# Kernel tuning notes

Measured on AMD Instinct MI355X. Metric: run time of the kernel, lower is better.

## Reference

```python
import jax, jax.numpy as jnp
import numpy as np

NSITES, NUP, NDN, BATCH = 256, 128, 128, 4096

def setup_inputs() -> dict:
    key = jax.random.key(0)
    k1, k2, k3, k4, k5 = jax.random.split(key, 5)
    phi_up = jax.random.normal(k1, (NSITES, NUP), dtype=jnp.float32)
    phi_dn = jax.random.normal(k2, (NSITES, NDN), dtype=jnp.float32)
    nfmodes = 2 * NSITES
    v = jax.random.normal(k3, (nfmodes, nfmodes), dtype=jnp.float32) / nfmodes
    # occupation: exactly NUP ones in first NSITES slots, NDN ones in last NSITES
    base_up = jnp.concatenate([jnp.ones(NUP, jnp.int32), jnp.zeros(NSITES - NUP, jnp.int32)])
    base_dn = jnp.concatenate([jnp.ones(NDN, jnp.int32), jnp.zeros(NSITES - NDN, jnp.int32)])
    n_up = jax.vmap(lambda k: jax.random.permutation(k, base_up))(jax.random.split(k4, BATCH))
    n_dn = jax.vmap(lambda k: jax.random.permutation(k, base_dn))(jax.random.split(k5, BATCH))
    n = jnp.concatenate([n_up, n_dn], axis=1)  # [B, 2*nsites]
    return {"n": n, "phi_up": phi_up, "phi_dn": phi_dn, "v": v}

def reference(n, phi_up, phi_dn, v):
    nsites, nup = phi_up.shape
    nf = n.astype(phi_up.dtype)                       # [B, 2*nsites]
    # Jastrow log factor: -0.5 * n @ v @ n  (sign is +1)
    log_j = -0.5 * jnp.einsum('bi,ij,bj->b', nf, v, nf)
    # fermion_idx: sorted indices of occupied modes, split by spin sector.
    # stable argsort of -n gives occupied indices in ascending order.
    idx_up = jnp.argsort(-n[:, :nsites], axis=1)[:, :nup]          # [B, nup]
    idx_dn = jnp.argsort(-n[:, nsites:], axis=1)[:, :phi_dn.shape[1]]
    M_up = phi_up[idx_up]                             # [B, nup, nup]
    M_dn = phi_dn[idx_dn]                             # [B, ndn, ndn]
    sign_up, logabs_up = jnp.linalg.slogdet(M_up)
    sign_dn, logabs_dn = jnp.linalg.slogdet(M_dn)
    sign = sign_up * sign_dn                          # jastrow sign is ones
    logabs = log_j + logabs_up + logabs_dn
    return jnp.stack([sign, logabs], axis=0)          # [2, B]
```

## Files before the change

kernel.cpp:

```cpp
#include <hip/hip_runtime.h>
#include <hip/hip_bf16.h>

#define NSITES 256
#define NM 128
#define NMODES 512

typedef unsigned long long u64;
typedef unsigned int u32;

#define REP8(M)    M(0) M(1) M(2) M(3) M(4) M(5) M(6) M(7)
#define REP8P(M,P) M(0,P) M(1,P) M(2,P) M(3,P) M(4,P) M(5,P) M(6,P) M(7,P)

template<int CTRL>
__device__ __forceinline__ float dpp_max(float x) {
  const int xi = __float_as_int(x);
  const int yi = __builtin_amdgcn_update_dpp(xi, xi, CTRL, 0xF, 0xF, false);
  return fmaxf(x, __int_as_float(yi));
}
__device__ __forceinline__ float wave_max(float x) {
  x = dpp_max<0x128>(x);
  x = dpp_max<0x124>(x);
  x = dpp_max<0x122>(x);
  x = dpp_max<0x121>(x);
  x = dpp_max<0x142>(x);
  x = dpp_max<0x143>(x);
  return __int_as_float(__builtin_amdgcn_readlane(__float_as_int(x), 63));
}

__global__ __launch_bounds__(256, 2) void lu_kernel(
    const int* __restrict__ n, const float* __restrict__ phi_up,
    const float* __restrict__ phi_dn, float* __restrict__ ws, int B)
{
  __shared__ int occ[NSITES];
  __shared__ int wcnt[4];
  __shared__ float colbuf[2][NM];
  __shared__ float rowP[2][NM];
  __shared__ int ipiv[NM];

  const int t = threadIdx.x;
  const int tx = t & 15, ty = t >> 4;
  const int lane = t & 63, wv = t >> 6;
  const int bs = blockIdx.x;
  const int b = bs >> 1, spin = bs & 1;
  const int* nn = n + b * NMODES + spin * NSITES;
  const float* phi = spin ? phi_dn : phi_up;

  {
    int v = nn[t];
    u64 m = __ballot(v != 0);
    if (lane == 0) wcnt[wv] = __popcll(m);
    __syncthreads();
    int off = 0;
    for (int w = 0; w < wv; ++w) off += wcnt[w];
    if (v) occ[off + __popcll(m & ((1ull << lane) - 1))] = t;
    __syncthreads();
  }

  float a[8][8];
#define GATH(II) { const float* pr_ = phi + occ[(II)*16 + ty] * NM; \
  a[II][0] = pr_[0*16+tx]; a[II][1] = pr_[1*16+tx]; \
  a[II][2] = pr_[2*16+tx]; a[II][3] = pr_[3*16+tx]; \
  a[II][4] = pr_[4*16+tx]; a[II][5] = pr_[5*16+tx]; \
  a[II][6] = pr_[6*16+tx]; a[II][7] = pr_[7*16+tx]; }
  REP8(GATH)
#undef GATH

  if (tx == 0) {
#define PUB0(II) colbuf[0][(II)*16 + ty] = a[II][0];
    REP8(PUB0)
#undef PUB0
  }
  if (tx == 1) {
#define PUB1(II) colbuf[1][(II)*16 + ty] = a[II][0];
    REP8(PUB1)
#undef PUB1
  }
  __syncthreads();

  float c1 = colbuf[0][lane];
  float c2 = colbuf[0][lane + 64];
  int r1 = 0, r2 = 0;
  float l2sum = 0.f;
  int sb = 0;
  const int bidx0 = (ty) << 2;
  const int bidx1 = (16 + ty) << 2;
  const int bidx2 = (32 + ty) << 2;
  const int bidx3 = (48 + ty) << 2;

  for (int k = 0; k < NM; ++k) {
    const int cur = k & 1;

    const float ca1 = r1 ? -1.0f : fabsf(c1);
    const float ca2 = r2 ? -1.0f : fabsf(c2);
    const float mx = wave_max(fmaxf(ca1, ca2));
    const u64 b1m = __ballot(ca1 == mx);
    const u64 b2m = __ballot(ca2 == mx);
    int p = b1m ? (__ffsll(b1m) - 1) : (__ffsll(b2m) + 63);
    p = __builtin_amdgcn_readfirstlane(p);
    const int pb = p >> 4, pt = p & 15, pl = p & 63;
    const float pivv = __int_as_float(
        p < 64 ? __builtin_amdgcn_readlane(__float_as_int(c1), pl)
               : __builtin_amdgcn_readlane(__float_as_int(c2), pl));
    const float rpiv = 1.0f / pivv;
    r1 |= (p == lane);
    r2 |= (p == lane + 64);
    const float m1 = r1 ? 0.f : c1 * rpiv;
    const float m2 = r2 ? 0.f : c2 * rpiv;

    if (ty == pt) {
      switch (pb) {
#define SRP(II) case II: \
  rowP[cur][0*16+tx]=a[II][0]; rowP[cur][1*16+tx]=a[II][1]; \
  rowP[cur][2*16+tx]=a[II][2]; rowP[cur][3*16+tx]=a[II][3]; \
  rowP[cur][4*16+tx]=a[II][4]; rowP[cur][5*16+tx]=a[II][5]; \
  rowP[cur][6*16+tx]=a[II][6]; rowP[cur][7*16+tx]=a[II][7]; break;
        REP8(SRP)
#undef SRP
      }
    }
    if (t == 0) ipiv[k] = p;
    l2sum += __log2f(mx);
    sb ^= (int)(__float_as_uint(pivv) >> 31);

    __syncthreads();

    if (k < NM - 1) {
      float mI[8];
#define BPM(II) mI[II] = __int_as_float(__builtin_amdgcn_ds_bpermute( \
    (II) < 4 ? ((II)==0?bidx0:(II)==1?bidx1:(II)==2?bidx2:bidx3) \
             : ((II)==4?bidx0:(II)==5?bidx1:(II)==6?bidx2:bidx3), \
    __float_as_int((II) < 4 ? m1 : m2)));
      REP8(BPM)
#undef BPM

      const int T = (k + 1) >> 4;
      float pr[8];
#define PRE(JJ, KB) if ((JJ) >= (KB)) pr[JJ] = rowP[cur][(JJ)*16 + tx];
#define UPDROW(II, KB) { \
  if (0 >= (KB)) a[II][0] = fmaf(-mI[II], pr[0], a[II][0]); \
  if (1 >= (KB)) a[II][1] = fmaf(-mI[II], pr[1], a[II][1]); \
  if (2 >= (KB)) a[II][2] = fmaf(-mI[II], pr[2], a[II][2]); \
  if (3 >= (KB)) a[II][3] = fmaf(-mI[II], pr[3], a[II][3]); \
  if (4 >= (KB)) a[II][4] = fmaf(-mI[II], pr[4], a[II][4]); \
  if (5 >= (KB)) a[II][5] = fmaf(-mI[II], pr[5], a[II][5]); \
  if (6 >= (KB)) a[II][6] = fmaf(-mI[II], pr[6], a[II][6]); \
  if (7 >= (KB)) a[II][7] = fmaf(-mI[II], pr[7], a[II][7]); }
#define LUCASE(KB) case KB: { REP8P(PRE, KB) REP8P(UPDROW, KB) } break;
      switch (T) {
        REP8(LUCASE)
      }
#undef LUCASE
#undef UPDROW
#undef PRE

      float d1 = colbuf[cur ^ 1][lane];
      float d2 = colbuf[cur ^ 1][lane + 64];
      const float ud = __int_as_float(
          p < 64 ? __builtin_amdgcn_readlane(__float_as_int(d1), pl)
                 : __builtin_amdgcn_readlane(__float_as_int(d2), pl));
      c1 = fmaf(-m1, ud, d1);
      c2 = fmaf(-m2, ud, d2);

      if (k < NM - 2) {
        const int cn = k + 2;
        if (tx == (cn & 15)) {
          switch (cn >> 4) {
#define PUBC(JJ) case JJ: \
  colbuf[cur][0*16+ty]=a[0][JJ]; colbuf[cur][1*16+ty]=a[1][JJ]; \
  colbuf[cur][2*16+ty]=a[2][JJ]; colbuf[cur][3*16+ty]=a[3][JJ]; \
  colbuf[cur][4*16+ty]=a[4][JJ]; colbuf[cur][5*16+ty]=a[5][JJ]; \
  colbuf[cur][6*16+ty]=a[6][JJ]; colbuf[cur][7*16+ty]=a[7][JJ]; break;
            REP8(PUBC)
#undef PUBC
          }
        }
      }
    }
  }

  __syncthreads();
  int inv = 0;
  if (t < NM) {
    const int my = ipiv[t];
    for (int l = t + 1; l < NM; ++l) inv += (my > ipiv[l]) ? 1 : 0;
  }
  const u64 bal = __ballot((t < NM) && (inv & 1));
  if (lane == 0) wcnt[wv] = __popcll(bal);
  __syncthreads();

  if (t == 0) {
    const int par = (wcnt[0] + wcnt[1] + wcnt[2] + wcnt[3]) & 1;
    const int s = (sb ^ par) & 1;
    ws[B + spin * B + b] = l2sum * 0.6931471805599453f;
    ws[3 * B + spin * B + b] = s ? -1.f : 1.f;
  }
}

__global__ __launch_bounds__(256) void jastrow_kernel(
    const int* __restrict__ n, const float* __restrict__ v,
    float* __restrict__ ws, int B)
{
  __shared__ int occ[256];
  __shared__ float nf[NMODES];
  __shared__ int wcnt[8];
  __shared__ float red[256];
  const int t = threadIdx.x, b = blockIdx.x;
  const int lane = t & 63, wv = t >> 6;
  const int* nn = n + b * NMODES;
  int v0 = nn[t], v1 = nn[256 + t];
  nf[t] = (float)v0;
  nf[256 + t] = (float)v1;
  u64 m0 = __ballot(v0 != 0), m1 = __ballot(v1 != 0);
  if (lane == 0) { wcnt[wv] = __popcll(m0); wcnt[4 + wv] = __popcll(m1); }
  __syncthreads();
  int off0 = 0;
  for (int w = 0; w < wv; ++w) off0 += wcnt[w];
  int base1 = wcnt[0] + wcnt[1] + wcnt[2] + wcnt[3];
  int off1 = base1;
  for (int w = 0; w < wv; ++w) off1 += wcnt[4 + w];
  if (v0) occ[off0 + __popcll(m0 & ((1ull << lane) - 1))] = t;
  if (v1) occ[off1 + __popcll(m1 & ((1ull << lane) - 1))] = 256 + t;
  __syncthreads();

  float acc = 0.f;
  for (int r = wv * 64; r < wv * 64 + 64; ++r) {
    const float* row = v + occ[r] * NMODES;
#pragma unroll
    for (int cc = 0; cc < 8; ++cc) {
      int c = cc * 64 + lane;
      acc += row[c] * nf[c];
    }
  }
  red[t] = acc;
  __syncthreads();
  for (int s = 128; s >= 1; s >>= 1) {
    if (t < s) red[t] += red[t + s];
    __syncthreads();
  }
  if (t == 0) ws[b] = -0.5f * red[0];
}

__global__ void finalize_kernel(const float* __restrict__ ws,
                                float* __restrict__ out, int B)
{
  int b = blockIdx.x * 256 + threadIdx.x;
  if (b < B) {
    float lj = ws[b];
    float la_u = ws[B + b], la_d = ws[2 * B + b];
    float s_u = ws[3 * B + b], s_d = ws[4 * B + b];
    out[b] = s_u * s_d;
    out[B + b] = lj + la_u + la_d;
  }
}

extern "C" void kernel_launch(void* const* d_in, const int* in_sizes, int n_in,
                              void* d_out, int out_size, void* d_ws, size_t ws_size,
                              hipStream_t stream) {
  const int* n = (const int*)d_in[0];
  const float* phi_up = (const float*)d_in[1];
  const float* phi_dn = (const float*)d_in[2];
  const float* v = (const float*)d_in[3];
  float* out = (float*)d_out;
  float* ws = (float*)d_ws;
  const int B = in_sizes[0] / NMODES;

  jastrow_kernel<<<B, 256, 0, stream>>>(n, v, ws, B);
  lu_kernel<<<2 * B, 256, 0, stream>>>(n, phi_up, phi_dn, ws, B);
  finalize_kernel<<<(B + 255) / 256, 256, 0, stream>>>(ws, out, B);
}
```

Baseline: 1.634 ms.

## Process two pivot columns per step in LU to halve block barriers

Restructures the per-matrix LU loop to factor two pivot steps per iteration: both pivots are chosen in registers from the two lookahead columns, the multipliers are corrected for the row coupling, and the trailing matrix gets a rank-2 update. This halves the number of __syncthreads and shared-memory round trips per factorization and fuses two FMA passes over the register tile. It adds extra bpermutes, readlanes and a deeper column lookahead, and uses the approximate rcp intrinsic instead of exact division for the pivot reciprocal, which may slightly change precision.

```diff
diff --git a/kernel.cpp b/kernel.cpp
--- a/kernel.cpp
+++ b/kernel.cpp
@@ -4,6 +4,7 @@
 #define NSITES 256
 #define NM 128
 #define NMODES 512
+#define NS 64
 
 typedef unsigned long long u64;
 typedef unsigned int u32;
@@ -26,6 +27,11 @@
   x = dpp_max<0x143>(x);
   return __int_as_float(__builtin_amdgcn_readlane(__float_as_int(x), 63));
 }
+__device__ __forceinline__ float rl2(float x1, float x2, int p) {
+  const int v1 = __builtin_amdgcn_readlane(__float_as_int(x1), p & 63);
+  const int v2 = __builtin_amdgcn_readlane(__float_as_int(x2), p & 63);
+  return __int_as_float(p < 64 ? v1 : v2);
+}
 
 __global__ __launch_bounds__(256, 2) void lu_kernel(
     const int* __restrict__ n, const float* __restrict__ phi_up,
@@ -33,8 +39,8 @@
 {
   __shared__ int occ[NSITES];
   __shared__ int wcnt[4];
-  __shared__ float colbuf[2][NM];
-  __shared__ float rowP[2][NM];
+  __shared__ float colbuf[2][2][NM];
+  __shared__ float rowP[2][2][NM];
   __shared__ int ipiv[NM];
 
   const int t = threadIdx.x;
@@ -65,20 +71,16 @@
   REP8(GATH)
 #undef GATH
 
-  if (tx == 0) {
-#define PUB0(II) colbuf[0][(II)*16 + ty] = a[II][0];
-    REP8(PUB0)
-#undef PUB0
-  }
-  if (tx == 1) {
-#define PUB1(II) colbuf[1][(II)*16 + ty] = a[II][0];
-    REP8(PUB1)
-#undef PUB1
-  }
-  __syncthreads();
-
-  float c1 = colbuf[0][lane];
-  float c2 = colbuf[0][lane + 64];
+#define PUBP(II, DST) DST[(II)*16 + ty] = a[II][0];
+  if (tx == 0) { float* d_ = &colbuf[1][0][0]; REP8P(PUBP, d_) }
+  if (tx == 1) { float* d_ = &colbuf[1][1][0]; REP8P(PUBP, d_) }
+  if (tx == 2) { float* d_ = &colbuf[0][0][0]; REP8P(PUBP, d_) }
+  if (tx == 3) { float* d_ = &colbuf[0][1][0]; REP8P(PUBP, d_) }
+#undef PUBP
+  __syncthreads();
+
+  float c1 = colbuf[1][0][lane], c2 = colbuf[1][0][lane + 64];
+  float d1 = colbuf[1][1][lane], d2 = colbuf[1][1][lane + 64];
   int r1 = 0, r2 = 0;
   float l2sum = 0.f;
   int sb = 0;
@@ -87,92 +89,127 @@
   const int bidx2 = (32 + ty) << 2;
   const int bidx3 = (48 + ty) << 2;
 
-  for (int k = 0; k < NM; ++k) {
-    const int cur = k & 1;
+  for (int s = 0; s < NS; ++s) {
+    const int pp = s & 1;
+    const int k0 = 2 * s;
 
     const float ca1 = r1 ? -1.0f : fabsf(c1);
     const float ca2 = r2 ? -1.0f : fabsf(c2);
-    const float mx = wave_max(fmaxf(ca1, ca2));
-    const u64 b1m = __ballot(ca1 == mx);
-    const u64 b2m = __ballot(ca2 == mx);
-    int p = b1m ? (__ffsll(b1m) - 1) : (__ffsll(b2m) + 63);
-    p = __builtin_amdgcn_readfirstlane(p);
-    const int pb = p >> 4, pt = p & 15, pl = p & 63;
-    const float pivv = __int_as_float(
-        p < 64 ? __builtin_amdgcn_readlane(__float_as_int(c1), pl)
-               : __builtin_amdgcn_readlane(__float_as_int(c2), pl));
-    const float rpiv = 1.0f / pivv;
-    r1 |= (p == lane);
-    r2 |= (p == lane + 64);
-    const float m1 = r1 ? 0.f : c1 * rpiv;
-    const float m2 = r2 ? 0.f : c2 * rpiv;
-
-    if (ty == pt) {
-      switch (pb) {
-#define SRP(II) case II: \
-  rowP[cur][0*16+tx]=a[II][0]; rowP[cur][1*16+tx]=a[II][1]; \
-  rowP[cur][2*16+tx]=a[II][2]; rowP[cur][3*16+tx]=a[II][3]; \
-  rowP[cur][4*16+tx]=a[II][4]; rowP[cur][5*16+tx]=a[II][5]; \
-  rowP[cur][6*16+tx]=a[II][6]; rowP[cur][7*16+tx]=a[II][7]; break;
-        REP8(SRP)
-#undef SRP
+    const float mx1 = wave_max(fmaxf(ca1, ca2));
+    const u64 A1 = __ballot(ca1 == mx1);
+    const u64 A2 = __ballot(ca2 == mx1);
+    int p1 = A1 ? (__ffsll(A1) - 1) : (__ffsll(A2) + 63);
+    p1 = __builtin_amdgcn_readfirstlane(p1);
+    const float piv1 = rl2(c1, c2, p1);
+    const float rp1 = __builtin_amdgcn_rcpf(piv1);
+    r1 |= (p1 == lane);
+    r2 |= (p1 == lane + 64);
+    const float m1a = r1 ? 0.f : c1 * rp1;
+    const float m1b = r2 ? 0.f : c2 * rp1;
+
+    const float ud = rl2(d1, d2, p1);
+    d1 = fmaf(-m1a, ud, d1);
+    d2 = fmaf(-m1b, ud, d2);
+
+    const float da1 = r1 ? -1.0f : fabsf(d1);
+    const float da2 = r2 ? -1.0f : fabsf(d2);
+    const float mx2 = wave_max(fmaxf(da1, da2));
+    const u64 B1 = __ballot(da1 == mx2);
+    const u64 B2 = __ballot(da2 == mx2);
+    int p2 = B1 ? (__ffsll(B1) - 1) : (__ffsll(B2) + 63);
+    p2 = __builtin_amdgcn_readfirstlane(p2);
+    const float piv2 = rl2(d1, d2, p2);
+    const float rp2 = __builtin_amdgcn_rcpf(piv2);
+    r1 |= (p2 == lane);
+    r2 |= (p2 == lane + 64);
+    const float m2a = r1 ? 0.f : d1 * rp2;
+    const float m2b = r2 ? 0.f : d2 * rp2;
+    const float mp = rl2(m1a, m1b, p2);
+
+    const int pb1 = p1 >> 4, pt1 = p1 & 15;
+    const int pb2 = p2 >> 4, pt2 = p2 & 15;
+#define SRX(II, DST) case II: \
+  DST[0*16+tx]=a[II][0]; DST[1*16+tx]=a[II][1]; DST[2*16+tx]=a[II][2]; DST[3*16+tx]=a[II][3]; \
+  DST[4*16+tx]=a[II][4]; DST[5*16+tx]=a[II][5]; DST[6*16+tx]=a[II][6]; DST[7*16+tx]=a[II][7]; break;
+    if (s < NS - 1) {
+      if (ty == pt1) {
+        float* d_ = &rowP[pp][0][0];
+        switch (pb1) { REP8P(SRX, d_) }
       }
-    }
-    if (t == 0) ipiv[k] = p;
-    l2sum += __log2f(mx);
-    sb ^= (int)(__float_as_uint(pivv) >> 31);
+      if (ty == pt2) {
+        float* d_ = &rowP[pp][1][0];
+        switch (pb2) { REP8P(SRX, d_) }
+      }
+    }
+#undef SRX
+    if (t == 0) { ipiv[k0] = p1; ipiv[k0 + 1] = p2; }
+    l2sum += __log2f(mx1) + __log2f(mx2);
+    sb ^= (int)((__float_as_uint(piv1) ^ __float_as_uint(piv2)) >> 31);
 
     __syncthreads();
-
-    if (k < NM - 1) {
-      float mI[8];
-#define BPM(II) mI[II] = __int_as_float(__builtin_amdgcn_ds_bpermute( \
-    (II) < 4 ? ((II)==0?bidx0:(II)==1?bidx1:(II)==2?bidx2:bidx3) \
-             : ((II)==4?bidx0:(II)==5?bidx1:(II)==6?bidx2:bidx3), \
-    __float_as_int((II) < 4 ? m1 : m2)));
-      REP8(BPM)
-#undef BPM
-
-      const int T = (k + 1) >> 4;
-      float pr[8];
-#define PRE(JJ, KB) if ((JJ) >= (KB)) pr[JJ] = rowP[cur][(JJ)*16 + tx];
-#define UPDROW(II, KB) { \
-  if (0 >= (KB)) a[II][0] = fmaf(-mI[II], pr[0], a[II][0]); \
-  if (1 >= (KB)) a[II][1] = fmaf(-mI[II], pr[1], a[II][1]); \
-  if (2 >= (KB)) a[II][2] = fmaf(-mI[II], pr[2], a[II][2]); \
-  if (3 >= (KB)) a[II][3] = fmaf(-mI[II], pr[3], a[II][3]); \
-  if (4 >= (KB)) a[II][4] = fmaf(-mI[II], pr[4], a[II][4]); \
-  if (5 >= (KB)) a[II][5] = fmaf(-mI[II], pr[5], a[II][5]); \
-  if (6 >= (KB)) a[II][6] = fmaf(-mI[II], pr[6], a[II][6]); \
-  if (7 >= (KB)) a[II][7] = fmaf(-mI[II], pr[7], a[II][7]); }
-#define LUCASE(KB) case KB: { REP8P(PRE, KB) REP8P(UPDROW, KB) } break;
-      switch (T) {
-        REP8(LUCASE)
-      }
-#undef LUCASE
-#undef UPDROW
-#undef PRE
-
-      float d1 = colbuf[cur ^ 1][lane];
-      float d2 = colbuf[cur ^ 1][lane + 64];
-      const float ud = __int_as_float(
-          p < 64 ? __builtin_amdgcn_readlane(__float_as_int(d1), pl)
-                 : __builtin_amdgcn_readlane(__float_as_int(d2), pl));
-      c1 = fmaf(-m1, ud, d1);
-      c2 = fmaf(-m2, ud, d2);
-
-      if (k < NM - 2) {
-        const int cn = k + 2;
-        if (tx == (cn & 15)) {
-          switch (cn >> 4) {
-#define PUBC(JJ) case JJ: \
-  colbuf[cur][0*16+ty]=a[0][JJ]; colbuf[cur][1*16+ty]=a[1][JJ]; \
-  colbuf[cur][2*16+ty]=a[2][JJ]; colbuf[cur][3*16+ty]=a[3][JJ]; \
-  colbuf[cur][4*16+ty]=a[4][JJ]; colbuf[cur][5*16+ty]=a[5][JJ]; \
-  colbuf[cur][6*16+ty]=a[6][JJ]; colbuf[cur][7*16+ty]=a[7][JJ]; break;
-            REP8(PUBC)
-#undef PUBC
-          }
+    if (s == NS - 1) break;
+
+    float mA[8], mB[8];
+#define BPA(II) mA[II] = __int_as_float(__builtin_amdgcn_ds_bpermute( \
+    ((II)&3)==0 ? bidx0 : ((II)&3)==1 ? bidx1 : ((II)&3)==2 ? bidx2 : bidx3, \
+    __float_as_int((II) < 4 ? m1a : m1b)));
+#define BPB(II) mB[II] = __int_as_float(__builtin_amdgcn_ds_bpermute( \
+    ((II)&3)==0 ? bidx0 : ((II)&3)==1 ? bidx1 : ((II)&3)==2 ? bidx2 : bidx3, \
+    __float_as_int((II) < 4 ? m2a : m2b)));
+    REP8(BPA)
+    REP8(BPB)
+#undef BPA
+#undef BPB
+#define CMP(II) mA[II] = fmaf(-mp, mB[II], mA[II]);
+    REP8(CMP)
+#undef CMP
+
+    const int T = (k0 + 2) >> 4;
+    float pr1[8], pr2[8];
+#define PRE2(JJ, KB) if ((JJ) >= (KB)) { \
+  pr1[JJ] = rowP[pp][0][(JJ)*16 + tx]; pr2[JJ] = rowP[pp][1][(JJ)*16 + tx]; }
+#define UPD2(II, KB) { \
+  if (0 >= (KB)) a[II][0] = fmaf(-mB[II], pr2[0], fmaf(-mA[II], pr1[0], a[II][0])); \
+  if (1 >= (KB)) a[II][1] = fmaf(-mB[II], pr2[1], fmaf(-mA[II], pr1[1], a[II][1])); \
+  if (2 >= (KB)) a[II][2] = fmaf(-mB[II], pr2[2], fmaf(-mA[II], pr1[2], a[II][2])); \
+  if (3 >= (KB)) a[II][3] = fmaf(-mB[II], pr2[3], fmaf(-mA[II], pr1[3], a[II][3])); \
+  if (4 >= (KB)) a[II][4] = fmaf(-mB[II], pr2[4], fmaf(-mA[II], pr1[4], a[II][4])); \
+  if (5 >= (KB)) a[II][5] = fmaf(-mB[II], pr2[5], fmaf(-mA[II], pr1[5], a[II][5])); \
+  if (6 >= (KB)) a[II][6] = fmaf(-mB[II], pr2[6], fmaf(-mA[II], pr1[6], a[II][6])); \
+  if (7 >= (KB)) a[II][7] = fmaf(-mB[II], pr2[7], fmaf(-mA[II], pr1[7], a[II][7])); }
+#define LUC2(KB) case KB: { REP8P(PRE2, KB) REP8P(UPD2, KB) } break;
+    switch (T) {
+      REP8(LUC2)
+    }
+#undef LUC2
+#undef UPD2
+#undef PRE2
+
+    {
+      float e1 = colbuf[pp][0][lane], e2 = colbuf[pp][0][lane + 64];
+      float u = rl2(e1, e2, p1);
+      e1 = fmaf(-m1a, u, e1); e2 = fmaf(-m1b, u, e2);
+      u = rl2(e1, e2, p2);
+      c1 = fmaf(-m2a, u, e1); c2 = fmaf(-m2b, u, e2);
+      float f1 = colbuf[pp][1][lane], f2 = colbuf[pp][1][lane + 64];
+      u = rl2(f1, f2, p1);
+      f1 = fmaf(-m1a, u, f1); f2 = fmaf(-m1b, u, f2);
+      u = rl2(f1, f2, p2);
+      d1 = fmaf(-m2a, u, f1); d2 = fmaf(-m2b, u, f2);
+    }
+
+    if (s <= NS - 3) {
+      const int j4 = k0 + 4;
+      const int c4l = j4 & 15;
+      const int sel = (tx == c4l) ? 0 : ((tx == c4l + 1) ? 1 : -1);
+      if (sel >= 0) {
+        float* dst = &colbuf[pp ^ 1][sel][0];
+        switch (j4 >> 4) {
+#define PUBJ(JJ) case JJ: \
+  dst[0*16+ty]=a[0][JJ]; dst[1*16+ty]=a[1][JJ]; dst[2*16+ty]=a[2][JJ]; dst[3*16+ty]=a[3][JJ]; \
+  dst[4*16+ty]=a[4][JJ]; dst[5*16+ty]=a[5][JJ]; dst[6*16+ty]=a[6][JJ]; dst[7*16+ty]=a[7][JJ]; break;
+          REP8(PUBJ)
+#undef PUBJ
         }
       }
     }
```

Result: slower. 1.739 ms (+6.4%).

## Split LU tile across 512 threads with 4x8 register tiles per thread

Applied to the files above, without the earlier changes.

Doubles the LU block to 512 threads so each thread owns a 4x8 sub-tile instead of 8x8. Row ownership, the pivot-row publish, the column publish and the multiplier ds_bpermute indexing are remapped to the 32-row thread layout, and launch bounds rise to 512,4. This halves per-thread FMA work and register pressure to expose more parallelism and occupancy. In exchange, each wave repeats the pivot search and every step needs wider barriers. The pivot reciprocal also switches to the hardware rcp approximation.

```diff
diff --git a/kernel.cpp b/kernel.cpp
--- a/kernel.cpp
+++ b/kernel.cpp
@@ -8,7 +8,9 @@
 typedef unsigned long long u64;
 typedef unsigned int u32;
 
+#define REP4(M)    M(0) M(1) M(2) M(3)
 #define REP8(M)    M(0) M(1) M(2) M(3) M(4) M(5) M(6) M(7)
+#define REP4P(M,P) M(0,P) M(1,P) M(2,P) M(3,P)
 #define REP8P(M,P) M(0,P) M(1,P) M(2,P) M(3,P) M(4,P) M(5,P) M(6,P) M(7,P)
 
 template<int CTRL>
@@ -26,13 +28,18 @@
   x = dpp_max<0x143>(x);
   return __int_as_float(__builtin_amdgcn_readlane(__float_as_int(x), 63));
 }
-
-__global__ __launch_bounds__(256, 2) void lu_kernel(
+__device__ __forceinline__ float rl2(float x1, float x2, int p) {
+  const int v1 = __builtin_amdgcn_readlane(__float_as_int(x1), p & 63);
+  const int v2 = __builtin_amdgcn_readlane(__float_as_int(x2), p & 63);
+  return __int_as_float(p < 64 ? v1 : v2);
+}
+
+__global__ __launch_bounds__(512, 4) void lu_kernel(
     const int* __restrict__ n, const float* __restrict__ phi_up,
     const float* __restrict__ phi_dn, float* __restrict__ ws, int B)
 {
   __shared__ int occ[NSITES];
-  __shared__ int wcnt[4];
+  __shared__ int wcnt[8];
   __shared__ float colbuf[2][NM];
   __shared__ float rowP[2][NM];
   __shared__ int ipiv[NM];
@@ -46,7 +53,7 @@
   const float* phi = spin ? phi_dn : phi_up;
 
   {
-    int v = nn[t];
+    int v = (t < NSITES) ? nn[t] : 0;
     u64 m = __ballot(v != 0);
     if (lane == 0) wcnt[wv] = __popcll(m);
     __syncthreads();
@@ -56,25 +63,19 @@
     __syncthreads();
   }
 
-  float a[8][8];
-#define GATH(II) { const float* pr_ = phi + occ[(II)*16 + ty] * NM; \
+  float a[4][8];
+#define GATH(II) { const float* pr_ = phi + occ[(II)*32 + ty] * NM; \
   a[II][0] = pr_[0*16+tx]; a[II][1] = pr_[1*16+tx]; \
   a[II][2] = pr_[2*16+tx]; a[II][3] = pr_[3*16+tx]; \
   a[II][4] = pr_[4*16+tx]; a[II][5] = pr_[5*16+tx]; \
   a[II][6] = pr_[6*16+tx]; a[II][7] = pr_[7*16+tx]; }
-  REP8(GATH)
+  REP4(GATH)
 #undef GATH
 
-  if (tx == 0) {
-#define PUB0(II) colbuf[0][(II)*16 + ty] = a[II][0];
-    REP8(PUB0)
-#undef PUB0
-  }
-  if (tx == 1) {
-#define PUB1(II) colbuf[1][(II)*16 + ty] = a[II][0];
-    REP8(PUB1)
-#undef PUB1
-  }
+#define PUBP(II, DST) DST[(II)*32 + ty] = a[II][0];
+  if (tx == 0) { float* d_ = &colbuf[0][0]; REP4P(PUBP, d_) }
+  if (tx == 1) { float* d_ = &colbuf[1][0]; REP4P(PUBP, d_) }
+#undef PUBP
   __syncthreads();
 
   float c1 = colbuf[0][lane];
@@ -82,10 +83,8 @@
   int r1 = 0, r2 = 0;
   float l2sum = 0.f;
   int sb = 0;
-  const int bidx0 = (ty) << 2;
-  const int bidx1 = (16 + ty) << 2;
-  const int bidx2 = (32 + ty) << 2;
-  const int bidx3 = (48 + ty) << 2;
+  const int bidxA = (ty) << 2;
+  const int bidxB = (32 + ty) << 2;
 
   for (int k = 0; k < NM; ++k) {
     const int cur = k & 1;
@@ -97,24 +96,20 @@
     const u64 b2m = __ballot(ca2 == mx);
     int p = b1m ? (__ffsll(b1m) - 1) : (__ffsll(b2m) + 63);
     p = __builtin_amdgcn_readfirstlane(p);
-    const int pb = p >> 4, pt = p & 15, pl = p & 63;
-    const float pivv = __int_as_float(
-        p < 64 ? __builtin_amdgcn_readlane(__float_as_int(c1), pl)
-               : __builtin_amdgcn_readlane(__float_as_int(c2), pl));
-    const float rpiv = 1.0f / pivv;
+    const float pivv = rl2(c1, c2, p);
+    const float rpiv = __builtin_amdgcn_rcpf(pivv);
     r1 |= (p == lane);
     r2 |= (p == lane + 64);
     const float m1 = r1 ? 0.f : c1 * rpiv;
     const float m2 = r2 ? 0.f : c2 * rpiv;
 
-    if (ty == pt) {
-      switch (pb) {
+    if (ty == (p & 31)) {
+      float* d_ = &rowP[cur][0];
+      switch (p >> 5) {
 #define SRP(II) case II: \
-  rowP[cur][0*16+tx]=a[II][0]; rowP[cur][1*16+tx]=a[II][1]; \
-  rowP[cur][2*16+tx]=a[II][2]; rowP[cur][3*16+tx]=a[II][3]; \
-  rowP[cur][4*16+tx]=a[II][4]; rowP[cur][5*16+tx]=a[II][5]; \
-  rowP[cur][6*16+tx]=a[II][6]; rowP[cur][7*16+tx]=a[II][7]; break;
-        REP8(SRP)
+  d_[0*16+tx]=a[II][0]; d_[1*16+tx]=a[II][1]; d_[2*16+tx]=a[II][2]; d_[3*16+tx]=a[II][3]; \
+  d_[4*16+tx]=a[II][4]; d_[5*16+tx]=a[II][5]; d_[6*16+tx]=a[II][6]; d_[7*16+tx]=a[II][7]; break;
+        REP4(SRP)
 #undef SRP
       }
     }
@@ -125,13 +120,11 @@
     __syncthreads();
 
     if (k < NM - 1) {
-      float mI[8];
-#define BPM(II) mI[II] = __int_as_float(__builtin_amdgcn_ds_bpermute( \
-    (II) < 4 ? ((II)==0?bidx0:(II)==1?bidx1:(II)==2?bidx2:bidx3) \
-             : ((II)==4?bidx0:(II)==5?bidx1:(II)==6?bidx2:bidx3), \
-    __float_as_int((II) < 4 ? m1 : m2)));
-      REP8(BPM)
-#undef BPM
+      float mI[4];
+      mI[0] = __int_as_float(__builtin_amdgcn_ds_bpermute(bidxA, __float_as_int(m1)));
+      mI[1] = __int_as_float(__builtin_amdgcn_ds_bpermute(bidxB, __float_as_int(m1)));
+      mI[2] = __int_as_float(__builtin_amdgcn_ds_bpermute(bidxA, __float_as_int(m2)));
+      mI[3] = __int_as_float(__builtin_amdgcn_ds_bpermute(bidxB, __float_as_int(m2)));
 
       const int T = (k + 1) >> 4;
       float pr[8];
@@ -145,7 +138,7 @@
   if (5 >= (KB)) a[II][5] = fmaf(-mI[II], pr[5], a[II][5]); \
   if (6 >= (KB)) a[II][6] = fmaf(-mI[II], pr[6], a[II][6]); \
   if (7 >= (KB)) a[II][7] = fmaf(-mI[II], pr[7], a[II][7]); }
-#define LUCASE(KB) case KB: { REP8P(PRE, KB) REP8P(UPDROW, KB) } break;
+#define LUCASE(KB) case KB: { REP8P(PRE, KB) REP4P(UPDROW, KB) } break;
       switch (T) {
         REP8(LUCASE)
       }
@@ -155,23 +148,20 @@
 
       float d1 = colbuf[cur ^ 1][lane];
       float d2 = colbuf[cur ^ 1][lane + 64];
-      const float ud = __int_as_float(
-          p < 64 ? __builtin_amdgcn_readlane(__float_as_int(d1), pl)
-                 : __builtin_amdgcn_readlane(__float_as_int(d2), pl));
+      const float ud = rl2(d1, d2, p);
       c1 = fmaf(-m1, ud, d1);
       c2 = fmaf(-m2, ud, d2);
 
       if (k < NM - 2) {
         const int cn = k + 2;
         if (tx == (cn & 15)) {
+          float* dst = &colbuf[cur][0];
           switch (cn >> 4) {
-#define PUBC(JJ) case JJ: \
-  colbuf[cur][0*16+ty]=a[0][JJ]; colbuf[cur][1*16+ty]=a[1][JJ]; \
-  colbuf[cur][2*16+ty]=a[2][JJ]; colbuf[cur][3*16+ty]=a[3][JJ]; \
-  colbuf[cur][4*16+ty]=a[4][JJ]; colbuf[cur][5*16+ty]=a[5][JJ]; \
-  colbuf[cur][6*16+ty]=a[6][JJ]; colbuf[cur][7*16+ty]=a[7][JJ]; break;
-            REP8(PUBC)
-#undef PUBC
+#define PUBJ(JJ) case JJ: \
+  dst[0*32+ty]=a[0][JJ]; dst[1*32+ty]=a[1][JJ]; \
+  dst[2*32+ty]=a[2][JJ]; dst[3*32+ty]=a[3][JJ]; break;
+            REP8(PUBJ)
+#undef PUBJ
           }
         }
       }
@@ -189,7 +179,8 @@
   __syncthreads();
 
   if (t == 0) {
-    const int par = (wcnt[0] + wcnt[1] + wcnt[2] + wcnt[3]) & 1;
+    int par = 0;
+    for (int w = 0; w < 8; ++w) par += wcnt[w];
     const int s = (sb ^ par) & 1;
     ws[B + spin * B + b] = l2sum * 0.6931471805599453f;
     ws[3 * B + spin * B + b] = s ? -1.f : 1.f;
@@ -265,6 +256,6 @@
   const int B = in_sizes[0] / NMODES;
 
   jastrow_kernel<<<B, 256, 0, stream>>>(n, v, ws, B);
-  lu_kernel<<<2 * B, 256, 0, stream>>>(n, phi_up, phi_dn, ws, B);
+  lu_kernel<<<2 * B, 512, 0, stream>>>(n, phi_up, phi_dn, ws, B);
   finalize_kernel<<<(B + 255) / 256, 256, 0, stream>>>(ws, out, B);
 }
```

Result: slower. 2.030 ms (+24.2%).
